# Performance work log

Hardware: AMD Instinct MI355X
Metric: run time of the kernel (lower is better)

## Reference

```python
import jax, jax.numpy as jnp
import numpy as np

N = 1_048_576   # collocation points
D_IN = 3        # seq_net[0]
H = 32          # hidden width (seq_net[1..3])
B = 4           # seq_net[-1] = number of parallel branches / outputs


def setup_inputs() -> dict:
    key = jax.random.key(0)
    ks = jax.random.split(key, 9)

    def init_w(k, shape, fan_in):
        bound = 1.0 / np.sqrt(fan_in)
        return jax.random.uniform(k, shape, jnp.float32, -bound, bound)

    x = jax.random.normal(ks[0], (N, D_IN), dtype=jnp.float32)
    # Per-branch weights stacked on leading branch axis B (torch.nn.Linear init ranges).
    W0 = init_w(ks[1], (B, D_IN, H), D_IN)
    b0 = init_w(ks[2], (B, H), D_IN)
    W1 = init_w(ks[3], (B, H, H), H)
    b1 = init_w(ks[4], (B, H), H)
    W2 = init_w(ks[5], (B, H, H), H)
    b2 = init_w(ks[6], (B, H), H)
    W3 = init_w(ks[7], (B, H, 1), H)
    b3 = init_w(ks[8], (B, 1), H)
    return {"x": x, "W0": W0, "b0": b0, "W1": W1, "b1": b1,
            "W2": W2, "b2": b2, "W3": W3, "b3": b3}


def reference(x, W0, b0, W1, b1, W2, b2, W3, b3):
    # All B branches computed as one batched GEMM chain (same math as the
    # python loop over per-branch Linear+tanh stacks in PFNN.forward).
    h = jnp.tanh(jnp.einsum('nd,bdh->bnh', x, W0) + b0[:, None, :])   # [B,N,H]
    h = jnp.tanh(jnp.einsum('bnd,bdh->bnh', h, W1) + b1[:, None, :])  # [B,N,H]
    h = jnp.tanh(jnp.einsum('bnd,bdh->bnh', h, W2) + b2[:, None, :])  # [B,N,H]
    out = jnp.einsum('bnd,bdh->bnh', h, W3) + b3[:, None, :]          # [B,N,1]
    # torch.cat(preds, dim=1): branch outputs side by side -> [N, B]
    return jnp.transpose(out[:, :, 0])
```

## Files before the change

kernel.cpp:

```cpp
#include <hip/hip_runtime.h>


#define NPTS 1048576
#define BLOCK 256
#define HROW 80
#define SCALE 2.8853900817779268f

#define OFF_BSC  16384
#define OFF_W0F  17408
#define OFF_B0P  25600
#define OFF_W3P  26112

using f16   = _Float16;
using f16x8 = __attribute__((ext_vector_type(8))) _Float16;
using f32x4 = __attribute__((ext_vector_type(4))) float;
using hfx2  = decltype(__builtin_amdgcn_cvt_pkrtz(0.0f, 0.0f));

__device__ __forceinline__ void inv4c(float v0, float v1, float v2, float v3,
                                      float& o0, float& o1, float& o2, float& o3)
{
    float a0 = __builtin_amdgcn_exp2f(v0) + 1.0f;
    float a1 = __builtin_amdgcn_exp2f(v1) + 1.0f;
    float a2 = __builtin_amdgcn_exp2f(v2) + 1.0f;
    float a3 = __builtin_amdgcn_exp2f(v3) + 1.0f;
    float p01 = a0 * a1;
    float p23 = a2 * a3;
    float p   = p01 * p23;
    float r   = __builtin_amdgcn_rcpf(p);
    float r01 = r * p23;
    float r23 = r * p01;
    o0 = __builtin_fmaf(r01, a1, -0.5f);
    o1 = __builtin_fmaf(r01, a0, -0.5f);
    o2 = __builtin_fmaf(r23, a3, -0.5f);
    o3 = __builtin_fmaf(r23, a2, -0.5f);
}

__device__ __forceinline__ void epi_mt(const f32x4& c0, const f32x4& c1, int mt,
                                       unsigned char* __restrict__ H,
                                       int col, int quad)
{
    #pragma unroll
    for (int r = 0; r < 4; r += 2) {
        int p = mt * 16 + quad * 4 + r;
        float o0, o1, o2, o3;
        inv4c(c0[r], c1[r], c0[r + 1], c1[r + 1], o0, o1, o2, o3);
        union { hfx2 h; unsigned int u; } cv0, cv1;
        cv0.h = __builtin_amdgcn_cvt_pkrtz(o0, o1);
        cv1.h = __builtin_amdgcn_cvt_pkrtz(o2, o3);
        *reinterpret_cast<unsigned int*>(H + p * HROW + 4 * col)       = cv0.u;
        *reinterpret_cast<unsigned int*>(H + (p + 1) * HROW + 4 * col) = cv1.u;
    }
}

__global__ void prep_kernel(const float* __restrict__ W0, const float* __restrict__ b0,
                            const float* __restrict__ W1, const float* __restrict__ b1,
                            const float* __restrict__ W2, const float* __restrict__ b2,
                            const float* __restrict__ W3,
                            unsigned char* __restrict__ ws)
{
    int i = blockIdx.x * 256 + threadIdx.x;
    if (i < 8192) {
        int k = i & 31, n = (i >> 5) & 15, t = (i >> 9) & 1, b = (i >> 10) & 3, l = i >> 12;
        int f = 2 * n + t;
        const float* W = l ? W2 : W1;
        reinterpret_cast<f16*>(ws)[i] = (f16)(-2.0f * SCALE * W[(b * 32 + k) * 32 + f]);
    } else if (i < 8448) {
        int j = i - 8192;
        int n = j & 15, t = (j >> 4) & 1, b = (j >> 5) & 3, l = j >> 7;
        const float* bb = l ? b2 : b1;
        reinterpret_cast<float*>(ws + OFF_BSC)[j] = SCALE * bb[b * 32 + 2 * n + t];
    } else if (i < 12544) {
        int j = i - 8448;
        int k = j & 31, n = (j >> 5) & 15, t = (j >> 9) & 1, b = (j >> 10) & 3;
        int f = 2 * n + t;
        int q = k >> 3, jj = k & 7;
        int row = -1; bool lo = false;
        if (q == 0 && jj < 6)      row = (jj < 3) ? jj : jj - 3;
        else if (q == 1 && jj < 3) { row = jj; lo = true; }
        f16 outv = (f16)0.0f;
        if (row >= 0) {
            float w  = SCALE * W0[(b * 3 + row) * 32 + f];
            f16   wh = (f16)w;
            outv = lo ? (f16)(w - (float)wh) : wh;
        }
        reinterpret_cast<f16*>(ws + OFF_W0F)[((b * 2 + t) * 16 + n) * 32 + k] = outv;
    } else if (i < 12672) {
        int j = i - 12544;
        int n = j & 15, t = (j >> 4) & 1, b = j >> 5;
        reinterpret_cast<float*>(ws + OFF_B0P)[(b * 2 + t) * 16 + n] = SCALE * b0[b * 32 + 2 * n + t];
    } else if (i < 12736) {
        int j = i - 12672;
        union { hfx2 h; unsigned int u; } cv;
        cv.h = __builtin_amdgcn_cvt_pkrtz(-2.0f * W3[2 * j], -2.0f * W3[2 * j + 1]);
        reinterpret_cast<unsigned int*>(ws + OFF_W3P)[j] = cv.u;
    }
}

__global__ __launch_bounds__(BLOCK, 8) void pfnn_kernel(
    const float* __restrict__ x, const unsigned char* __restrict__ ws,
    const float* __restrict__ b3,
    float* __restrict__ out)
{
    __shared__ __align__(16) unsigned char Hl[4][64 * HROW];

    const f16*   Wf  = reinterpret_cast<const f16*>(ws);
    const float* Bsc = reinterpret_cast<const float*>(ws + OFF_BSC);
    const f16*   W0f = reinterpret_cast<const f16*>(ws + OFF_W0F);
    const float* B0p = reinterpret_cast<const float*>(ws + OFF_B0P);
    const unsigned int* W3p = reinterpret_cast<const unsigned int*>(ws + OFF_W3P);

    const int t    = threadIdx.x;
    const int lane = t & 63;
    const int wv   = t >> 6;
    const int col  = lane & 15;
    const int quad = lane >> 4;
    unsigned char* __restrict__ H = &Hl[wv][0];

    const int n0 = blockIdx.x * BLOCK + t;
    const float x0 = x[3 * n0 + 0];
    const float x1 = x[3 * n0 + 1];
    const float x2 = x[3 * n0 + 2];

    f16x8 xfrag[4];
    {
        union { hfx2 h; int u; } q0_, q1_, q2_;
        q0_.h = __builtin_amdgcn_cvt_pkrtz(x0, x1);
        float r0 = x0 - (float)q0_.h[0];
        float r1 = x1 - (float)q0_.h[1];
        q1_.h = __builtin_amdgcn_cvt_pkrtz(x2, r0);
        float r2 = x2 - (float)q1_.h[0];
        q2_.h = __builtin_amdgcn_cvt_pkrtz(r1, r2);
        int d0 = q0_.u, d1 = q1_.u, d2 = q2_.u;
        #pragma unroll
        for (int mt = 0; mt < 4; ++mt) {
            int addr = 4 * (mt * 16 + col);
            union { int i[4]; f16x8 f; } u;
            u.i[0] = __builtin_amdgcn_ds_bpermute(addr, d0);
            u.i[1] = __builtin_amdgcn_ds_bpermute(addr, d1);
            u.i[2] = __builtin_amdgcn_ds_bpermute(addr, d2);
            u.i[3] = 0;
            xfrag[mt] = u.f;
        }
    }

    float res[4];

    #pragma unroll 1
    for (int b = 0; b < 4; ++b) {
        {
            const f16* wb = W0f + (b * 2) * 512;
            f16x8 bf0 = *reinterpret_cast<const f16x8*>(wb + col * 32 + quad * 8);
            f16x8 bf1 = *reinterpret_cast<const f16x8*>(wb + 512 + col * 32 + quad * 8);
            float bias0 = B0p[(b * 2 + 0) * 16 + col];
            float bias1 = B0p[(b * 2 + 1) * 16 + col];
            f32x4 ci0 = {bias0, bias0, bias0, bias0};
            f32x4 ci1 = {bias1, bias1, bias1, bias1};

            #pragma unroll
            for (int mt = 0; mt < 4; ++mt) {
                f32x4 c0 = __builtin_amdgcn_mfma_f32_16x16x32_f16(xfrag[mt], bf0, ci0, 0, 0, 0);
                f32x4 c1 = __builtin_amdgcn_mfma_f32_16x16x32_f16(xfrag[mt], bf1, ci1, 0, 0, 0);
                epi_mt(c0, c1, mt, H, col, quad);
            }
        }

        #pragma unroll
        for (int l = 0; l < 2; ++l) {
            const f16* wb = Wf + ((l * 4 + b) * 2) * 512;
            f16x8 bf0 = *reinterpret_cast<const f16x8*>(wb + col * 32 + quad * 8);
            f16x8 bf1 = *reinterpret_cast<const f16x8*>(wb + 512 + col * 32 + quad * 8);
            float bias0 = Bsc[((l * 4 + b) * 2 + 0) * 16 + col];
            float bias1 = Bsc[((l * 4 + b) * 2 + 1) * 16 + col];
            f32x4 ci0 = {bias0, bias0, bias0, bias0};
            f32x4 ci1 = {bias1, bias1, bias1, bias1};

            #pragma unroll
            for (int mt = 0; mt < 4; ++mt) {
                const f16x8 av = *reinterpret_cast<const f16x8*>(
                    H + (mt * 16 + col) * HROW + quad * 16);
                f32x4 c0 = __builtin_amdgcn_mfma_f32_16x16x32_f16(av, bf0, ci0, 0, 0, 0);
                f32x4 c1 = __builtin_amdgcn_mfma_f32_16x16x32_f16(av, bf1, ci1, 0, 0, 0);
                epi_mt(c0, c1, mt, H, col, quad);
            }
        }

        {
            float o = b3[b];
            const unsigned char* row = H + lane * HROW;
            const unsigned int* w3p = W3p + b * 16;
            #pragma unroll
            for (int i = 0; i < 4; ++i) {
                uint4 u = *reinterpret_cast<const uint4*>(row + 16 * i);
#if __has_builtin(__builtin_amdgcn_fdot2)
                union { unsigned int uu; hfx2 hh; } h0, h1, h2, h3, w0, w1, w2, w3u;
                h0.uu = u.x; h1.uu = u.y; h2.uu = u.z; h3.uu = u.w;
                w0.uu = w3p[4 * i];     w1.uu = w3p[4 * i + 1];
                w2.uu = w3p[4 * i + 2]; w3u.uu = w3p[4 * i + 3];
                o = __builtin_amdgcn_fdot2(h0.hh, w0.hh, o, false);
                o = __builtin_amdgcn_fdot2(h1.hh, w1.hh, o, false);
                o = __builtin_amdgcn_fdot2(h2.hh, w2.hh, o, false);
                o = __builtin_amdgcn_fdot2(h3.hh, w3u.hh, o, false);
#else
                union { unsigned int uu; f16 h[2]; } hh[4], wwu[4];
                hh[0].uu = u.x; hh[1].uu = u.y; hh[2].uu = u.z; hh[3].uu = u.w;
                #pragma unroll
                for (int q = 0; q < 4; ++q) {
                    wwu[q].uu = w3p[4 * i + q];
                    o = __builtin_fmaf((float)hh[q].h[0], (float)wwu[q].h[0], o);
                    o = __builtin_fmaf((float)hh[q].h[1], (float)wwu[q].h[1], o);
                }
#endif
            }
            res[b] = o;
        }
    }

    float4 r4 = make_float4(res[0], res[1], res[2], res[3]);
    *reinterpret_cast<float4*>(out + 4 * n0) = r4;
}

extern "C" void kernel_launch(void* const* d_in, const int* in_sizes, int n_in,
                              void* d_out, int out_size, void* d_ws, size_t ws_size,
                              hipStream_t stream) {
    const float* x  = (const float*)d_in[0];
    const float* W0 = (const float*)d_in[1];
    const float* b0 = (const float*)d_in[2];
    const float* W1 = (const float*)d_in[3];
    const float* b1 = (const float*)d_in[4];
    const float* W2 = (const float*)d_in[5];
    const float* b2 = (const float*)d_in[6];
    const float* W3 = (const float*)d_in[7];
    const float* b3 = (const float*)d_in[8];
    float* out = (float*)d_out;
    unsigned char* ws = (unsigned char*)d_ws;

    prep_kernel<<<dim3(50), dim3(256), 0, stream>>>(W0, b0, W1, b1, W2, b2, W3, ws);
    pfnn_kernel<<<dim3(NPTS / BLOCK), dim3(BLOCK), 0, stream>>>(x, ws, b3, out);
}
```

Before: 152.0 us.

## Keep hidden activations in registers via transposed MFMA chaining

Swaps the MFMA operand roles so weights form the A operand and activations the B operand. The f16 tanh output of one layer can then be packed straight into the next layer's B fragment in registers, with no LDS round trip. The layer-0 bias is folded into the x fragment through a constant-one element, and the final dot product is reduced across quads with shuffles. Results are staged in a small LDS buffer before a vectorized store. In exchange, loops now run over 16-point tiles with unroll 1, which gives less instruction-level parallelism per wave and adds more weight loads from global memory.

```diff
diff --git a/kernel.cpp b/kernel.cpp
--- a/kernel.cpp
+++ b/kernel.cpp
@@ -3,13 +3,13 @@
 
 #define NPTS 1048576
 #define BLOCK 256
-#define HROW 80
+#define NWAVE 4
 #define SCALE 2.8853900817779268f
 
-#define OFF_BSC  16384
-#define OFF_W0F  17408
-#define OFF_B0P  25600
-#define OFF_W3P  26112
+#define OFF_W0A 0
+#define OFF_WHA 8192
+#define OFF_BT  24576
+#define OFF_W3T 25600
 
 using f16   = _Float16;
 using f16x8 = __attribute__((ext_vector_type(8))) _Float16;
@@ -35,21 +35,32 @@
     o3 = __builtin_fmaf(r23, a2, -0.5f);
 }
 
-__device__ __forceinline__ void epi_mt(const f32x4& c0, const f32x4& c1, int mt,
-                                       unsigned char* __restrict__ H,
-                                       int col, int quad)
-{
-    #pragma unroll
-    for (int r = 0; r < 4; r += 2) {
-        int p = mt * 16 + quad * 4 + r;
-        float o0, o1, o2, o3;
-        inv4c(c0[r], c1[r], c0[r + 1], c1[r + 1], o0, o1, o2, o3);
-        union { hfx2 h; unsigned int u; } cv0, cv1;
-        cv0.h = __builtin_amdgcn_cvt_pkrtz(o0, o1);
-        cv1.h = __builtin_amdgcn_cvt_pkrtz(o2, o3);
-        *reinterpret_cast<unsigned int*>(H + p * HROW + 4 * col)       = cv0.u;
-        *reinterpret_cast<unsigned int*>(H + (p + 1) * HROW + 4 * col) = cv1.u;
-    }
+__device__ __forceinline__ void tanh_pack(const f32x4& ca, const f32x4& cb, uint4& u)
+{
+    float o0, o1, o2, o3, p0, p1, p2, p3;
+    inv4c(ca[0], ca[1], ca[2], ca[3], o0, o1, o2, o3);
+    inv4c(cb[0], cb[1], cb[2], cb[3], p0, p1, p2, p3);
+    union { hfx2 h; unsigned int w; } c0, c1, c2, c3;
+    c0.h = __builtin_amdgcn_cvt_pkrtz(o0, o1);
+    c1.h = __builtin_amdgcn_cvt_pkrtz(o2, o3);
+    c2.h = __builtin_amdgcn_cvt_pkrtz(p0, p1);
+    c3.h = __builtin_amdgcn_cvt_pkrtz(p2, p3);
+    u.x = c0.w; u.y = c1.w; u.z = c2.w; u.w = c3.w;
+}
+
+__device__ __forceinline__ float fdot2w(unsigned int a, unsigned int b, float acc)
+{
+#if __has_builtin(__builtin_amdgcn_fdot2)
+    union { unsigned int u; hfx2 h; } A, B;
+    A.u = a; B.u = b;
+    return __builtin_amdgcn_fdot2(A.h, B.h, acc, false);
+#else
+    union { unsigned int u; f16 h[2]; } A, B;
+    A.u = a; B.u = b;
+    acc = __builtin_fmaf((float)A.h[0], (float)B.h[0], acc);
+    acc = __builtin_fmaf((float)A.h[1], (float)B.h[1], acc);
+    return acc;
+#endif
 }
 
 __global__ void prep_kernel(const float* __restrict__ W0, const float* __restrict__ b0,
@@ -59,40 +70,50 @@
                             unsigned char* __restrict__ ws)
 {
     int i = blockIdx.x * 256 + threadIdx.x;
-    if (i < 8192) {
-        int k = i & 31, n = (i >> 5) & 15, t = (i >> 9) & 1, b = (i >> 10) & 3, l = i >> 12;
-        int f = 2 * n + t;
+    if (i < 4096) {
+        int e = i & 7, lane = (i >> 3) & 63, half = (i >> 9) & 1, b = i >> 10;
+        int q = lane >> 4, c = lane & 15;
+        int f = half * 16 + c;
+        f16 r = (f16)0.0f;
+        if (q == 0) {
+            if (e < 6) {
+                int row = (e < 3) ? e : e - 3;
+                r = (f16)(SCALE * W0[(b * 3 + row) * 32 + f]);
+            } else if (e == 6) {
+                r = (f16)(SCALE * b0[b * 32 + f]);
+            }
+        } else if (q == 1) {
+            if (e < 3) {
+                float w = SCALE * W0[(b * 3 + e) * 32 + f];
+                f16 wh = (f16)w;
+                r = (f16)(w - (float)wh);
+            } else if (e == 6) {
+                float w = SCALE * b0[b * 32 + f];
+                f16 wh = (f16)w;
+                r = (f16)(w - (float)wh);
+            }
+        }
+        reinterpret_cast<f16*>(ws + OFF_W0A)[i] = r;
+    } else if (i < 12288) {
+        int j = i - 4096;
+        int e = j & 7, lane = (j >> 3) & 63, half = (j >> 9) & 1, b = (j >> 10) & 3, l = j >> 12;
+        int q = lane >> 4, c = lane & 15;
+        int k = (e < 4) ? (4 * q + e) : (16 + 4 * q + (e - 4));
+        int f = half * 16 + c;
         const float* W = l ? W2 : W1;
-        reinterpret_cast<f16*>(ws)[i] = (f16)(-2.0f * SCALE * W[(b * 32 + k) * 32 + f]);
-    } else if (i < 8448) {
-        int j = i - 8192;
-        int n = j & 15, t = (j >> 4) & 1, b = (j >> 5) & 3, l = j >> 7;
+        reinterpret_cast<f16*>(ws + OFF_WHA)[j] = (f16)(-2.0f * SCALE * W[(b * 32 + k) * 32 + f]);
+    } else if (i < 12544) {
+        int j = i - 12288;
+        int r = j & 3, q = (j >> 2) & 3, half = (j >> 4) & 1, b = (j >> 5) & 3, l = j >> 7;
         const float* bb = l ? b2 : b1;
-        reinterpret_cast<float*>(ws + OFF_BSC)[j] = SCALE * bb[b * 32 + 2 * n + t];
-    } else if (i < 12544) {
-        int j = i - 8448;
-        int k = j & 31, n = (j >> 5) & 15, t = (j >> 9) & 1, b = (j >> 10) & 3;
-        int f = 2 * n + t;
-        int q = k >> 3, jj = k & 7;
-        int row = -1; bool lo = false;
-        if (q == 0 && jj < 6)      row = (jj < 3) ? jj : jj - 3;
-        else if (q == 1 && jj < 3) { row = jj; lo = true; }
-        f16 outv = (f16)0.0f;
-        if (row >= 0) {
-            float w  = SCALE * W0[(b * 3 + row) * 32 + f];
-            f16   wh = (f16)w;
-            outv = lo ? (f16)(w - (float)wh) : wh;
-        }
-        reinterpret_cast<f16*>(ws + OFF_W0F)[((b * 2 + t) * 16 + n) * 32 + k] = outv;
-    } else if (i < 12672) {
+        reinterpret_cast<float*>(ws + OFF_BT)[j] = SCALE * bb[b * 32 + half * 16 + 4 * q + r];
+    } else if (i < 12608) {
         int j = i - 12544;
-        int n = j & 15, t = (j >> 4) & 1, b = j >> 5;
-        reinterpret_cast<float*>(ws + OFF_B0P)[(b * 2 + t) * 16 + n] = SCALE * b0[b * 32 + 2 * n + t];
-    } else if (i < 12736) {
-        int j = i - 12672;
+        int jj = j & 3, q = (j >> 2) & 3, b = j >> 4;
+        int k0 = (jj < 2) ? (4 * q + 2 * jj) : (16 + 4 * q + 2 * (jj - 2));
         union { hfx2 h; unsigned int u; } cv;
-        cv.h = __builtin_amdgcn_cvt_pkrtz(-2.0f * W3[2 * j], -2.0f * W3[2 * j + 1]);
-        reinterpret_cast<unsigned int*>(ws + OFF_W3P)[j] = cv.u;
+        cv.h = __builtin_amdgcn_cvt_pkrtz(-2.0f * W3[b * 32 + k0], -2.0f * W3[b * 32 + k0 + 1]);
+        reinterpret_cast<unsigned int*>(ws + OFF_W3T)[j] = cv.u;
     }
 }
 
@@ -101,27 +122,25 @@
     const float* __restrict__ b3,
     float* __restrict__ out)
 {
-    __shared__ __align__(16) unsigned char Hl[4][64 * HROW];
-
-    const f16*   Wf  = reinterpret_cast<const f16*>(ws);
-    const float* Bsc = reinterpret_cast<const float*>(ws + OFF_BSC);
-    const f16*   W0f = reinterpret_cast<const f16*>(ws + OFF_W0F);
-    const float* B0p = reinterpret_cast<const float*>(ws + OFF_B0P);
-    const unsigned int* W3p = reinterpret_cast<const unsigned int*>(ws + OFF_W3P);
+    __shared__ __align__(16) float resL[NWAVE][256];
+
+    const f16* W0A = reinterpret_cast<const f16*>(ws + OFF_W0A);
+    const f16* WHA = reinterpret_cast<const f16*>(ws + OFF_WHA);
+    const float* BT = reinterpret_cast<const float*>(ws + OFF_BT);
+    const unsigned int* W3T = reinterpret_cast<const unsigned int*>(ws + OFF_W3T);
 
     const int t    = threadIdx.x;
     const int lane = t & 63;
     const int wv   = t >> 6;
     const int col  = lane & 15;
     const int quad = lane >> 4;
-    unsigned char* __restrict__ H = &Hl[wv][0];
 
     const int n0 = blockIdx.x * BLOCK + t;
     const float x0 = x[3 * n0 + 0];
     const float x1 = x[3 * n0 + 1];
     const float x2 = x[3 * n0 + 2];
 
-    f16x8 xfrag[4];
+    int d0, d1, d2;
     {
         union { hfx2 h; int u; } q0_, q1_, q2_;
         q0_.h = __builtin_amdgcn_cvt_pkrtz(x0, x1);
@@ -130,92 +149,57 @@
         q1_.h = __builtin_amdgcn_cvt_pkrtz(x2, r0);
         float r2 = x2 - (float)q1_.h[0];
         q2_.h = __builtin_amdgcn_cvt_pkrtz(r1, r2);
-        int d0 = q0_.u, d1 = q1_.u, d2 = q2_.u;
-        #pragma unroll
-        for (int mt = 0; mt < 4; ++mt) {
-            int addr = 4 * (mt * 16 + col);
-            union { int i[4]; f16x8 f; } u;
-            u.i[0] = __builtin_amdgcn_ds_bpermute(addr, d0);
-            u.i[1] = __builtin_amdgcn_ds_bpermute(addr, d1);
-            u.i[2] = __builtin_amdgcn_ds_bpermute(addr, d2);
-            u.i[3] = 0;
-            xfrag[mt] = u.f;
+        d0 = q0_.u; d1 = q1_.u; d2 = q2_.u;
+    }
+
+    #pragma unroll 1
+    for (int mt = 0; mt < 4; ++mt) {
+        int addr = 4 * (mt * 16 + col);
+        union { int i[4]; f16x8 f; } xu;
+        xu.i[0] = __builtin_amdgcn_ds_bpermute(addr, d0);
+        xu.i[1] = __builtin_amdgcn_ds_bpermute(addr, d1);
+        xu.i[2] = __builtin_amdgcn_ds_bpermute(addr, d2);
+        xu.i[3] = 0x00003C00;
+        const f16x8 xf = xu.f;
+
+        #pragma unroll 1
+        for (int b = 0; b < 4; ++b) {
+            const f16* w0b = W0A + ((b * 2) * 64 + lane) * 8;
+            const f16x8 a00 = *reinterpret_cast<const f16x8*>(w0b);
+            const f16x8 a01 = *reinterpret_cast<const f16x8*>(w0b + 512);
+            const f32x4 cz = {0.0f, 0.0f, 0.0f, 0.0f};
+            f32x4 v0 = __builtin_amdgcn_mfma_f32_16x16x32_f16(a00, xf, cz, 0, 0, 0);
+            f32x4 v1 = __builtin_amdgcn_mfma_f32_16x16x32_f16(a01, xf, cz, 0, 0, 0);
+            union { uint4 u; f16x8 f; } h;
+            tanh_pack(v0, v1, h.u);
+
+            #pragma unroll
+            for (int l = 0; l < 2; ++l) {
+                const f16* wb = WHA + (((l * 4 + b) * 2) * 64 + lane) * 8;
+                const f16x8 a0 = *reinterpret_cast<const f16x8*>(wb);
+                const f16x8 a1 = *reinterpret_cast<const f16x8*>(wb + 512);
+                const f32x4 bt0 = *reinterpret_cast<const f32x4*>(
+                    BT + ((l * 4 + b) * 2 + 0) * 16 + quad * 4);
+                const f32x4 bt1 = *reinterpret_cast<const f32x4*>(
+                    BT + ((l * 4 + b) * 2 + 1) * 16 + quad * 4);
+                f32x4 n0v = __builtin_amdgcn_mfma_f32_16x16x32_f16(a0, h.f, bt0, 0, 0, 0);
+                f32x4 n1v = __builtin_amdgcn_mfma_f32_16x16x32_f16(a1, h.f, bt1, 0, 0, 0);
+                tanh_pack(n0v, n1v, h.u);
+            }
+
+            const uint4 w3v = *reinterpret_cast<const uint4*>(W3T + (b * 4 + quad) * 4);
+            float s = (quad == 0) ? b3[b] : 0.0f;
+            s = fdot2w(h.u.x, w3v.x, s);
+            s = fdot2w(h.u.y, w3v.y, s);
+            s = fdot2w(h.u.z, w3v.z, s);
+            s = fdot2w(h.u.w, w3v.w, s);
+            s += __shfl_xor(s, 16);
+            s += __shfl_xor(s, 32);
+            if (quad == mt) resL[wv][lane * 4 + b] = s;
         }
     }
 
-    float res[4];
-
-    #pragma unroll 1
-    for (int b = 0; b < 4; ++b) {
-        {
-            const f16* wb = W0f + (b * 2) * 512;
-            f16x8 bf0 = *reinterpret_cast<const f16x8*>(wb + col * 32 + quad * 8);
-            f16x8 bf1 = *reinterpret_cast<const f16x8*>(wb + 512 + col * 32 + quad * 8);
-            float bias0 = B0p[(b * 2 + 0) * 16 + col];
-            float bias1 = B0p[(b * 2 + 1) * 16 + col];
-            f32x4 ci0 = {bias0, bias0, bias0, bias0};
-            f32x4 ci1 = {bias1, bias1, bias1, bias1};
-
-            #pragma unroll
-            for (int mt = 0; mt < 4; ++mt) {
-                f32x4 c0 = __builtin_amdgcn_mfma_f32_16x16x32_f16(xfrag[mt], bf0, ci0, 0, 0, 0);
-                f32x4 c1 = __builtin_amdgcn_mfma_f32_16x16x32_f16(xfrag[mt], bf1, ci1, 0, 0, 0);
-                epi_mt(c0, c1, mt, H, col, quad);
-            }
-        }
-
-        #pragma unroll
-        for (int l = 0; l < 2; ++l) {
-            const f16* wb = Wf + ((l * 4 + b) * 2) * 512;
-            f16x8 bf0 = *reinterpret_cast<const f16x8*>(wb + col * 32 + quad * 8);
-            f16x8 bf1 = *reinterpret_cast<const f16x8*>(wb + 512 + col * 32 + quad * 8);
-            float bias0 = Bsc[((l * 4 + b) * 2 + 0) * 16 + col];
-            float bias1 = Bsc[((l * 4 + b) * 2 + 1) * 16 + col];
-            f32x4 ci0 = {bias0, bias0, bias0, bias0};
-            f32x4 ci1 = {bias1, bias1, bias1, bias1};
-
-            #pragma unroll
-            for (int mt = 0; mt < 4; ++mt) {
-                const f16x8 av = *reinterpret_cast<const f16x8*>(
-                    H + (mt * 16 + col) * HROW + quad * 16);
-                f32x4 c0 = __builtin_amdgcn_mfma_f32_16x16x32_f16(av, bf0, ci0, 0, 0, 0);
-                f32x4 c1 = __builtin_amdgcn_mfma_f32_16x16x32_f16(av, bf1, ci1, 0, 0, 0);
-                epi_mt(c0, c1, mt, H, col, quad);
-            }
-        }
-
-        {
-            float o = b3[b];
-            const unsigned char* row = H + lane * HROW;
-            const unsigned int* w3p = W3p + b * 16;
-            #pragma unroll
-            for (int i = 0; i < 4; ++i) {
-                uint4 u = *reinterpret_cast<const uint4*>(row + 16 * i);
-#if __has_builtin(__builtin_amdgcn_fdot2)
-                union { unsigned int uu; hfx2 hh; } h0, h1, h2, h3, w0, w1, w2, w3u;
-                h0.uu = u.x; h1.uu = u.y; h2.uu = u.z; h3.uu = u.w;
-                w0.uu = w3p[4 * i];     w1.uu = w3p[4 * i + 1];
-                w2.uu = w3p[4 * i + 2]; w3u.uu = w3p[4 * i + 3];
-                o = __builtin_amdgcn_fdot2(h0.hh, w0.hh, o, false);
-                o = __builtin_amdgcn_fdot2(h1.hh, w1.hh, o, false);
-                o = __builtin_amdgcn_fdot2(h2.hh, w2.hh, o, false);
-                o = __builtin_amdgcn_fdot2(h3.hh, w3u.hh, o, false);
-#else
-                union { unsigned int uu; f16 h[2]; } hh[4], wwu[4];
-                hh[0].uu = u.x; hh[1].uu = u.y; hh[2].uu = u.z; hh[3].uu = u.w;
-                #pragma unroll
-                for (int q = 0; q < 4; ++q) {
-                    wwu[q].uu = w3p[4 * i + q];
-                    o = __builtin_fmaf((float)hh[q].h[0], (float)wwu[q].h[0], o);
-                    o = __builtin_fmaf((float)hh[q].h[1], (float)wwu[q].h[1], o);
-                }
-#endif
-            }
-            res[b] = o;
-        }
-    }
-
-    float4 r4 = make_float4(res[0], res[1], res[2], res[3]);
+    const float4 r4 = *reinterpret_cast<const float4*>(&resL[wv][lane * 4]);
     *reinterpret_cast<float4*>(out + 4 * n0) = r4;
 }
 
```

After: 165.6 us. 1.09x slower.
